# Performance work log

Hardware: AMD Instinct MI355X
Metric: run time of the kernel (lower is better)

Reference implementation:

```python
import jax, jax.numpy as jnp
import numpy as np

N = 100000        # num nodes
E = 1600000       # num edges (no self loops; added inside reference)
F_IN = 501        # dataset.num_features + 1
H1, C1 = 8, 8     # conv1: heads=8, out_channels=8 (concat -> 64)
NCLS = 40         # conv2: heads=1, out_channels=num_classes, concat=False
NEG_SLOPE = 0.2


def _glorot(key, shape):
    fan_in, fan_out = shape[-2] if len(shape) > 1 else shape[-1], shape[-1]
    lim = np.sqrt(6.0 / (fan_in + fan_out)).astype(np.float32)
    return jax.random.uniform(key, shape, jnp.float32, -lim, lim)


def setup_inputs() -> dict:
    key = jax.random.key(0)
    ks = jax.random.split(key, 10)
    x = jax.random.normal(ks[0], (N, F_IN), jnp.float32)
    # random edges guaranteed to have src != dst (PyG removes self loops then re-adds)
    src = jax.random.randint(ks[1], (E,), 0, N)
    off = jax.random.randint(ks[2], (E,), 1, N)
    dst = (src + off) % N
    edge_index = jnp.stack([src, dst]).astype(jnp.int32)
    W1 = _glorot(ks[3], (F_IN, H1 * C1))
    att_src1 = _glorot(ks[4], (H1, C1))
    att_dst1 = _glorot(ks[5], (H1, C1))
    W2 = _glorot(ks[6], (H1 * C1, NCLS))
    att_src2 = _glorot(ks[7], (1, NCLS))
    att_dst2 = _glorot(ks[8], (1, NCLS))
    bias2 = jnp.zeros((NCLS,), jnp.float32)
    return {"x": x, "W1": W1, "att_src1": att_src1, "att_dst1": att_dst1,
            "W2": W2, "att_src2": att_src2, "att_dst2": att_dst2,
            "bias2": bias2, "edge_index": edge_index, "idx": 0}


def _gat_conv(x2d, W, att_s, att_d, src, dst, heads, C, sign, concat, bias):
    n = x2d.shape[0]
    # linear projection (shared lin_src == lin_dst for int in_channels)
    xh = (x2d @ W).reshape(n, heads, C)                       # [N,H,C]
    a_src = jnp.sum(xh * (sign * att_s), axis=-1)             # [N,H]
    a_dst = jnp.sum(xh * (sign * att_d), axis=-1)             # [N,H]
    # add self loops
    ar = jnp.arange(n, dtype=src.dtype)
    src = jnp.concatenate([src, ar])
    dst = jnp.concatenate([dst, ar])
    # per-edge attention logits + leaky relu
    alpha = a_src[src] + a_dst[dst]                           # [E',H]
    alpha = jax.nn.leaky_relu(alpha, NEG_SLOPE)
    # segment softmax grouped by destination node
    m = jax.ops.segment_max(alpha, dst, num_segments=n)       # [N,H]
    e = jnp.exp(alpha - m[dst])
    denom = jax.ops.segment_sum(e, dst, num_segments=n)       # [N,H]
    a = e / (denom[dst] + 1e-16)                              # [E',H]
    # scatter-add aggregation of weighted source features
    out = jax.ops.segment_sum(xh[src] * a[:, :, None], dst, num_segments=n)  # [N,H,C]
    out = out.reshape(n, heads * C) if concat else out.mean(axis=1)
    if bias is not None:
        out = out + bias
    return out


def reference(x, W1, att_src1, att_dst1, W2, att_src2, att_dst2, bias2, edge_index, idx):
    sign = -1.0 if idx == 1 else 1.0
    src, dst = edge_index[0], edge_index[1]
    h = _gat_conv(x, W1, att_src1, att_dst1, src, dst, H1, C1, sign, True, None)
    h = jax.nn.elu(h)
    out = _gat_conv(h, W2, att_src2, att_dst2, src, dst, 1, NCLS, sign, False, bias2)
    return out
```

## Files before the change

### kernel.cpp

```cpp
#include <hip/hip_runtime.h>

#define N_NODES 100000
#define N_EDGES 1600000
#define F_IN    501
#define H1      8
#define C1      8
#define D1      64
#define NCLS    40

#define BSH     9
#define NBUCK   196
#define BINBLK  256

typedef __attribute__((ext_vector_type(8))) short bf16x8;
typedef __attribute__((ext_vector_type(4))) float f32x4;

__device__ __forceinline__ float lrelu(float x) { return x > 0.f ? x : 0.2f * x; }

__device__ __forceinline__ unsigned short f2bf(float f) {
    unsigned u = __float_as_uint(f);
    u += 0x7FFFu + ((u >> 16) & 1u);
    return (unsigned short)(u >> 16);
}
__device__ __forceinline__ float bf2f(unsigned short u) {
    return __uint_as_float(((unsigned)u) << 16);
}

__global__ __launch_bounds__(512) void gemm1(const float* __restrict__ x,
                                             const float* __restrict__ W1,
                                             unsigned short* __restrict__ xh1b) {
    __shared__ unsigned short Bs[64 * 512];

    const int tid = threadIdx.x;

    for (int i = tid; i < F_IN * 64; i += 512) {
        int k = i >> 6, n = i & 63;
        int byte = (n << 10) + (k << 1);
        byte ^= (n & 7) << 4;
        Bs[byte >> 1] = f2bf(W1[i]);
    }
    if (tid < 64) {
        #pragma unroll
        for (int k = F_IN; k < 512; ++k) {
            int byte = (tid << 10) + (k << 1);
            byte ^= (tid & 7) << 4;
            Bs[byte >> 1] = 0;
        }
    }
    __syncthreads();

    const int lane = tid & 63;
    const int wave = tid >> 6;
    const int lr   = lane & 15;
    const int hi   = lane >> 4;
    const int lk   = hi * 8;

    const int row  = blockIdx.x * 128 + wave * 16 + lr;
    const int rowc = row < N_NODES ? row : N_NODES - 1;
    const float* aptr = x + (size_t)rowc * F_IN + lk;

    f32x4 acc[4] = {};
    float av[4][8];

    #pragma unroll
    for (int pf = 0; pf < 4; ++pf)
        #pragma unroll
        for (int j = 0; j < 8; ++j)
            av[pf][j] = aptr[pf * 32 + j];

    #pragma unroll
    for (int s = 0; s < 16; ++s) {
        bf16x8 a;
        #pragma unroll
        for (int j = 0; j < 8; ++j) a[j] = (short)f2bf(av[s & 3][j]);

        if (s + 4 < 15) {
            #pragma unroll
            for (int j = 0; j < 8; ++j)
                av[s & 3][j] = aptr[(s + 4) * 32 + j];
        } else if (s + 4 == 15) {
            #pragma unroll
            for (int j = 0; j < 8; ++j) {
                int k = 15 * 32 + lk + j;
                av[s & 3][j] = (k < F_IN) ? aptr[15 * 32 + j] : 0.f;
            }
        }

        #pragma unroll
        for (int n = 0; n < 4; ++n) {
            int c = n * 16 + lr;
            int byte = (c << 10) + ((s * 32 + lk) << 1);
            byte ^= (c & 7) << 4;
            bf16x8 b = *(const bf16x8*)((const char*)Bs + byte);
            acc[n] = __builtin_amdgcn_mfma_f32_16x16x32_bf16(a, b, acc[n], 0, 0, 0);
        }
    }

    int rbase = blockIdx.x * 128 + wave * 16 + hi * 4;
    #pragma unroll
    for (int n = 0; n < 4; ++n) {
        int col = n * 16 + lr;
        #pragma unroll
        for (int r = 0; r < 4; ++r) {
            int grow = rbase + r;
            if (grow < N_NODES) xh1b[(size_t)grow * D1 + col] = f2bf(acc[n][r]);
        }
    }
}

__global__ void a1k(const unsigned short* __restrict__ xh1b,
                    const float* __restrict__ att_s, const float* __restrict__ att_d,
                    const int* __restrict__ idxp,
                    float* __restrict__ a_src, float* __restrict__ a_dst) {
    int gid = blockIdx.x * blockDim.x + threadIdx.x;
    if (gid >= N_NODES * H1) return;
    int n = gid >> 3, h = gid & 7;
    float sign = (idxp[0] == 1) ? -1.f : 1.f;
    uint4 u = *(const uint4*)(xh1b + (size_t)n * D1 + h * C1);
    float v[8];
    v[0] = bf2f((unsigned short)(u.x & 0xffff)); v[1] = bf2f((unsigned short)(u.x >> 16));
    v[2] = bf2f((unsigned short)(u.y & 0xffff)); v[3] = bf2f((unsigned short)(u.y >> 16));
    v[4] = bf2f((unsigned short)(u.z & 0xffff)); v[5] = bf2f((unsigned short)(u.z >> 16));
    v[6] = bf2f((unsigned short)(u.w & 0xffff)); v[7] = bf2f((unsigned short)(u.w >> 16));
    float ss = 0.f, sd = 0.f;
    #pragma unroll
    for (int c = 0; c < C1; ++c) {
        ss += v[c] * att_s[h * C1 + c];
        sd += v[c] * att_d[h * C1 + c];
    }
    a_src[gid] = sign * ss;
    a_dst[gid] = sign * sd;
}

__global__ __launch_bounds__(256) void bc1(const int* __restrict__ ei,
                                           int* __restrict__ gcnt) {
    __shared__ int h[NBUCK];
    for (int i = threadIdx.x; i < NBUCK; i += 256) h[i] = 0;
    __syncthreads();
    for (int e = blockIdx.x * 256 + threadIdx.x; e < N_EDGES; e += BINBLK * 256)
        atomicAdd(&h[ei[N_EDGES + e] >> BSH], 1);
    __syncthreads();
    for (int i = threadIdx.x; i < NBUCK; i += 256)
        if (h[i]) atomicAdd(&gcnt[i], h[i]);
}

__global__ __launch_bounds__(256) void bc2(const int* __restrict__ gcnt,
                                           int* __restrict__ bbase,
                                           int* __restrict__ bcur,
                                           int* __restrict__ rowptr) {
    __shared__ int s[256];
    int t = threadIdx.x;
    int v = (t < NBUCK) ? gcnt[t] : 0;
    s[t] = v;
    __syncthreads();
    for (int off = 1; off < 256; off <<= 1) {
        int x = 0;
        if (t >= off) x = s[t - off];
        __syncthreads();
        if (t >= off) s[t] += x;
        __syncthreads();
    }
    if (t < NBUCK) { int e = s[t] - v; bbase[t] = e; bcur[t] = e; }
    if (t == 0)    { bbase[NBUCK] = N_EDGES; rowptr[N_NODES] = N_EDGES; }
}

__global__ __launch_bounds__(256) void bc3(const int* __restrict__ ei,
                                           int* __restrict__ bcur,
                                           unsigned* __restrict__ tmp) {
    __shared__ int h[NBUCK];
    __shared__ int base[NBUCK];
    for (int i = threadIdx.x; i < NBUCK; i += 256) h[i] = 0;
    __syncthreads();
    for (int e = blockIdx.x * 256 + threadIdx.x; e < N_EDGES; e += BINBLK * 256)
        atomicAdd(&h[ei[N_EDGES + e] >> BSH], 1);
    __syncthreads();
    for (int i = threadIdx.x; i < NBUCK; i += 256) {
        int c = h[i];
        base[i] = c ? atomicAdd(&bcur[i], c) : 0;
        h[i] = 0;
    }
    __syncthreads();
    for (int e = blockIdx.x * 256 + threadIdx.x; e < N_EDGES; e += BINBLK * 256) {
        int s = ei[e], d = ei[N_EDGES + e];
        int b = d >> BSH;
        int r = atomicAdd(&h[b], 1);
        tmp[base[b] + r] = ((unsigned)s << BSH) | (unsigned)(d & 511);
    }
}

__global__ __launch_bounds__(256) void bc4(const unsigned* __restrict__ tmp,
                                           const int* __restrict__ bbase,
                                           int* __restrict__ rowptr,
                                           int* __restrict__ ssrc) {
    __shared__ int cnt[512], ofs[512], sc[256];
    const int b = blockIdx.x, t = threadIdx.x;
    const int lo = bbase[b], hi = bbase[b + 1];
    cnt[t] = 0; cnt[t + 256] = 0;
    __syncthreads();
    for (int i = lo + t; i < hi; i += 256)
        atomicAdd(&cnt[tmp[i] & 511], 1);
    __syncthreads();
    int v0 = cnt[2 * t], v1 = cnt[2 * t + 1];
    int sum = v0 + v1;
    sc[t] = sum;
    __syncthreads();
    for (int off = 1; off < 256; off <<= 1) {
        int x = 0;
        if (t >= off) x = sc[t - off];
        __syncthreads();
        if (t >= off) sc[t] += x;
        __syncthreads();
    }
    int pre = sc[t] - sum;
    int n0 = (b << BSH) + 2 * t;
    int base0 = lo + pre, base1 = base0 + v0;
    if (n0 < N_NODES)     rowptr[n0]     = base0;
    if (n0 + 1 < N_NODES) rowptr[n0 + 1] = base1;
    ofs[2 * t] = base0; ofs[2 * t + 1] = base1;
    __syncthreads();
    for (int i = lo + t; i < hi; i += 256) {
        unsigned v = tmp[i];
        int p = atomicAdd(&ofs[v & 511], 1);
        ssrc[p] = (int)(v >> BSH);
    }
}

__global__ __launch_bounds__(256) void agg1(const int* __restrict__ rowptr,
                                            const int* __restrict__ ssrc,
                                            const unsigned short* __restrict__ xh1b,
                                            const float* __restrict__ a_src,
                                            const float* __restrict__ a_dst,
                                            unsigned short* __restrict__ hb) {
    int wid  = (blockIdx.x * 256 + threadIdx.x) >> 6;
    int lane = threadIdx.x & 63;
    if (wid >= N_NODES) return;
    const int d  = wid;
    const int li = lane & 15;
    const int q  = lane >> 4;
    const int hh = li >> 1;

    const float adh = a_dst[d * H1 + hh];
    float a0 = 0.f, a1 = 0.f, a2 = 0.f, a3 = 0.f, den = 0.f;
    if (q == 0) {
        float e0 = __expf(lrelu(a_src[d * H1 + hh] + adh));
        ushort4 v = *(const ushort4*)&xh1b[(size_t)d * D1 + (li << 2)];
        a0 = e0 * bf2f(v.x); a1 = e0 * bf2f(v.y);
        a2 = e0 * bf2f(v.z); a3 = e0 * bf2f(v.w);
        den = e0;
    }

    const int beg = rowptr[d], end = rowptr[d + 1];
    for (int p = beg + q; p < end; p += 4) {
        int s = ssrc[p];
        float e = __expf(lrelu(a_src[s * H1 + hh] + adh));
        ushort4 v = *(const ushort4*)&xh1b[(size_t)s * D1 + (li << 2)];
        a0 = fmaf(e, bf2f(v.x), a0);
        a1 = fmaf(e, bf2f(v.y), a1);
        a2 = fmaf(e, bf2f(v.z), a2);
        a3 = fmaf(e, bf2f(v.w), a3);
        den += e;
    }

    a0 += __shfl_xor(a0, 16); a0 += __shfl_xor(a0, 32);
    a1 += __shfl_xor(a1, 16); a1 += __shfl_xor(a1, 32);
    a2 += __shfl_xor(a2, 16); a2 += __shfl_xor(a2, 32);
    a3 += __shfl_xor(a3, 16); a3 += __shfl_xor(a3, 32);
    den += __shfl_xor(den, 16); den += __shfl_xor(den, 32);

    if (lane < 16) {
        float inv = 1.f / (den + 1e-16f);
        float v0 = a0 * inv, v1 = a1 * inv, v2 = a2 * inv, v3 = a3 * inv;
        v0 = v0 > 0.f ? v0 : (__expf(v0) - 1.f);
        v1 = v1 > 0.f ? v1 : (__expf(v1) - 1.f);
        v2 = v2 > 0.f ? v2 : (__expf(v2) - 1.f);
        v3 = v3 > 0.f ? v3 : (__expf(v3) - 1.f);
        ushort4 r;
        r.x = f2bf(v0); r.y = f2bf(v1); r.z = f2bf(v2); r.w = f2bf(v3);
        *(ushort4*)&hb[(size_t)d * D1 + (li << 2)] = r;
    }
}

__global__ void gemm2(const unsigned short* __restrict__ hb,
                      const float* __restrict__ W2,
                      unsigned short* __restrict__ xh2b) {
    int gid = blockIdx.x * blockDim.x + threadIdx.x;
    if (gid >= N_NODES * NCLS) return;
    int n = gid / NCLS, c = gid % NCLS;
    const uint4* hr = (const uint4*)(hb + (size_t)n * D1);
    float s = 0.f;
    #pragma unroll
    for (int q = 0; q < 8; ++q) {
        uint4 u = hr[q];
        int k = q * 8;
        s = fmaf(bf2f((unsigned short)(u.x & 0xffff)), W2[(k + 0) * NCLS + c], s);
        s = fmaf(bf2f((unsigned short)(u.x >> 16)),    W2[(k + 1) * NCLS + c], s);
        s = fmaf(bf2f((unsigned short)(u.y & 0xffff)), W2[(k + 2) * NCLS + c], s);
        s = fmaf(bf2f((unsigned short)(u.y >> 16)),    W2[(k + 3) * NCLS + c], s);
        s = fmaf(bf2f((unsigned short)(u.z & 0xffff)), W2[(k + 4) * NCLS + c], s);
        s = fmaf(bf2f((unsigned short)(u.z >> 16)),    W2[(k + 5) * NCLS + c], s);
        s = fmaf(bf2f((unsigned short)(u.w & 0xffff)), W2[(k + 6) * NCLS + c], s);
        s = fmaf(bf2f((unsigned short)(u.w >> 16)),    W2[(k + 7) * NCLS + c], s);
    }
    xh2b[gid] = f2bf(s);
}

__global__ void a2k(const unsigned short* __restrict__ xh2b,
                    const float* __restrict__ att_s2, const float* __restrict__ att_d2,
                    const int* __restrict__ idxp,
                    float* __restrict__ a_src2, float* __restrict__ a_dst2) {
    int n = blockIdx.x * blockDim.x + threadIdx.x;
    if (n >= N_NODES) return;
    float sign = (idxp[0] == 1) ? -1.f : 1.f;
    const uint4* xr = (const uint4*)(xh2b + (size_t)n * NCLS);
    float ss = 0.f, sd = 0.f;
    #pragma unroll
    for (int q = 0; q < 5; ++q) {
        uint4 u = xr[q];
        int k = q * 8;
        float v[8];
        v[0] = bf2f((unsigned short)(u.x & 0xffff)); v[1] = bf2f((unsigned short)(u.x >> 16));
        v[2] = bf2f((unsigned short)(u.y & 0xffff)); v[3] = bf2f((unsigned short)(u.y >> 16));
        v[4] = bf2f((unsigned short)(u.z & 0xffff)); v[5] = bf2f((unsigned short)(u.z >> 16));
        v[6] = bf2f((unsigned short)(u.w & 0xffff)); v[7] = bf2f((unsigned short)(u.w >> 16));
        #pragma unroll
        for (int j = 0; j < 8; ++j) {
            ss += v[j] * att_s2[k + j];
            sd += v[j] * att_d2[k + j];
        }
    }
    a_src2[n] = sign * ss;
    a_dst2[n] = sign * sd;
}

__global__ __launch_bounds__(256) void agg2(const int* __restrict__ rowptr,
                                            const int* __restrict__ ssrc,
                                            const unsigned short* __restrict__ xh2b,
                                            const float* __restrict__ a_src2,
                                            const float* __restrict__ a_dst2,
                                            const float* __restrict__ bias2,
                                            float* __restrict__ out) {
    int wid  = (blockIdx.x * 256 + threadIdx.x) >> 6;
    int lane = threadIdx.x & 63;
    if (wid >= N_NODES) return;
    const int d  = wid;
    const int li = lane & 15;
    const int q  = lane >> 4;
    const bool act = li < (NCLS / 4);

    const float adh = a_dst2[d];
    float a0 = 0.f, a1 = 0.f, a2 = 0.f, a3 = 0.f, den = 0.f;
    if (q == 0) {
        float e0 = __expf(lrelu(a_src2[d] + adh));
        if (act) {
            ushort4 v = *(const ushort4*)&xh2b[(size_t)d * NCLS + (li << 2)];
            a0 = e0 * bf2f(v.x); a1 = e0 * bf2f(v.y);
            a2 = e0 * bf2f(v.z); a3 = e0 * bf2f(v.w);
        }
        den = e0;
    }

    const int beg = rowptr[d], end = rowptr[d + 1];
    for (int p = beg + q; p < end; p += 4) {
        int s = ssrc[p];
        float e = __expf(lrelu(a_src2[s] + adh));
        if (act) {
            ushort4 v = *(const ushort4*)&xh2b[(size_t)s * NCLS + (li << 2)];
            a0 = fmaf(e, bf2f(v.x), a0);
            a1 = fmaf(e, bf2f(v.y), a1);
            a2 = fmaf(e, bf2f(v.z), a2);
            a3 = fmaf(e, bf2f(v.w), a3);
        }
        den += e;
    }

    a0 += __shfl_xor(a0, 16); a0 += __shfl_xor(a0, 32);
    a1 += __shfl_xor(a1, 16); a1 += __shfl_xor(a1, 32);
    a2 += __shfl_xor(a2, 16); a2 += __shfl_xor(a2, 32);
    a3 += __shfl_xor(a3, 16); a3 += __shfl_xor(a3, 32);
    den += __shfl_xor(den, 16); den += __shfl_xor(den, 32);

    if (lane < 16 && act) {
        float inv = 1.f / (den + 1e-16f);
        float4 bv = *(const float4*)&bias2[li << 2];
        float4 r;
        r.x = a0 * inv + bv.x;
        r.y = a1 * inv + bv.y;
        r.z = a2 * inv + bv.z;
        r.w = a3 * inv + bv.w;
        *(float4*)&out[(size_t)d * NCLS + (li << 2)] = r;
    }
}

extern "C" void kernel_launch(void* const* d_in, const int* in_sizes, int n_in,
                              void* d_out, int out_size, void* d_ws, size_t ws_size,
                              hipStream_t stream) {
    const float* x    = (const float*)d_in[0];
    const float* W1   = (const float*)d_in[1];
    const float* as1w = (const float*)d_in[2];
    const float* ad1w = (const float*)d_in[3];
    const float* W2   = (const float*)d_in[4];
    const float* as2w = (const float*)d_in[5];
    const float* ad2w = (const float*)d_in[6];
    const float* b2   = (const float*)d_in[7];
    const int*   ei   = (const int*)d_in[8];
    const int*   idxp = (const int*)d_in[9];
    float* out = (float*)d_out;

    unsigned short* xh1b = (unsigned short*)d_ws;
    unsigned short* hb   = xh1b + (size_t)N_NODES * D1;
    unsigned short* xh2b = hb + (size_t)N_NODES * D1;
    float* as1 = (float*)(xh2b + (size_t)N_NODES * NCLS);
    float* ad1 = as1 + (size_t)N_NODES * H1;
    float* as2 = ad1 + (size_t)N_NODES * H1;
    float* ad2 = as2 + N_NODES;
    int* gcnt   = (int*)(ad2 + N_NODES);
    int* bbase  = gcnt + NBUCK;
    int* bcur   = bbase + (NBUCK + 1);
    int* rowptr = bcur + NBUCK;
    unsigned* tmp = (unsigned*)(rowptr + (N_NODES + 1));
    int* ssrc   = (int*)(tmp + N_EDGES);

    hipMemsetAsync(gcnt, 0, (size_t)NBUCK * sizeof(int), stream);
    bc1<<<BINBLK, 256, 0, stream>>>(ei, gcnt);
    bc2<<<1, 256, 0, stream>>>(gcnt, bbase, bcur, rowptr);
    bc3<<<BINBLK, 256, 0, stream>>>(ei, bcur, tmp);
    bc4<<<NBUCK, 256, 0, stream>>>(tmp, bbase, rowptr, ssrc);

    gemm1<<<(N_NODES + 127) / 128, 512, 0, stream>>>(x, W1, xh1b);
    a1k<<<(N_NODES * H1 + 255) / 256, 256, 0, stream>>>(xh1b, as1w, ad1w, idxp, as1, ad1);
    agg1<<<(N_NODES * 64 + 255) / 256, 256, 0, stream>>>(rowptr, ssrc, xh1b, as1, ad1, hb);

    gemm2<<<(N_NODES * NCLS + 255) / 256, 256, 0, stream>>>(hb, W2, xh2b);
    a2k<<<(N_NODES + 255) / 256, 256, 0, stream>>>(xh2b, as2w, ad2w, idxp, as2, ad2);
    agg2<<<(N_NODES * 64 + 255) / 256, 256, 0, stream>>>(rowptr, ssrc, xh2b, as2, ad2, b2, out);
}
```

Measured before the change: 336.2 us.

## Partition node features into channel planes and aggregate each plane in separate passes

```diff
diff --git a/kernel.cpp b/kernel.cpp
--- a/kernel.cpp
+++ b/kernel.cpp
@@ -28,7 +28,7 @@
 
 __global__ __launch_bounds__(512) void gemm1(const float* __restrict__ x,
                                              const float* __restrict__ W1,
-                                             unsigned short* __restrict__ xh1b) {
+                                             unsigned short* __restrict__ xh1p) {
     __shared__ unsigned short Bs[64 * 512];
 
     const int tid = threadIdx.x;
@@ -99,24 +99,28 @@
     int rbase = blockIdx.x * 128 + wave * 16 + hi * 4;
     #pragma unroll
     for (int n = 0; n < 4; ++n) {
-        int col = n * 16 + lr;
+        unsigned short* dst = xh1p + (size_t)n * N_NODES * 16;
         #pragma unroll
         for (int r = 0; r < 4; ++r) {
             int grow = rbase + r;
-            if (grow < N_NODES) xh1b[(size_t)grow * D1 + col] = f2bf(acc[n][r]);
+            if (grow < N_NODES) dst[(size_t)grow * 16 + lr] = f2bf(acc[n][r]);
         }
     }
 }
 
-__global__ void a1k(const unsigned short* __restrict__ xh1b,
+__global__ void a1k(const unsigned short* __restrict__ xh1p,
                     const float* __restrict__ att_s, const float* __restrict__ att_d,
                     const int* __restrict__ idxp,
-                    float* __restrict__ a_src, float* __restrict__ a_dst) {
+                    float* __restrict__ asP, float* __restrict__ adP) {
     int gid = blockIdx.x * blockDim.x + threadIdx.x;
-    if (gid >= N_NODES * H1) return;
-    int n = gid >> 3, h = gid & 7;
+    if (gid >= 4 * 2 * N_NODES) return;
+    int p   = gid / (2 * N_NODES);
+    int r   = gid - p * (2 * N_NODES);
+    int n   = r >> 1, sub = r & 1;
+    int h   = 2 * p + sub;
     float sign = (idxp[0] == 1) ? -1.f : 1.f;
-    uint4 u = *(const uint4*)(xh1b + (size_t)n * D1 + h * C1);
+    const unsigned short* row = xh1p + (size_t)p * N_NODES * 16 + n * 16 + sub * 8;
+    uint4 u = *(const uint4*)row;
     float v[8];
     v[0] = bf2f((unsigned short)(u.x & 0xffff)); v[1] = bf2f((unsigned short)(u.x >> 16));
     v[2] = bf2f((unsigned short)(u.y & 0xffff)); v[3] = bf2f((unsigned short)(u.y >> 16));
@@ -124,12 +128,12 @@
     v[6] = bf2f((unsigned short)(u.w & 0xffff)); v[7] = bf2f((unsigned short)(u.w >> 16));
     float ss = 0.f, sd = 0.f;
     #pragma unroll
-    for (int c = 0; c < C1; ++c) {
+    for (int c = 0; c < 8; ++c) {
         ss += v[c] * att_s[h * C1 + c];
         sd += v[c] * att_d[h * C1 + c];
     }
-    a_src[gid] = sign * ss;
-    a_dst[gid] = sign * sd;
+    asP[gid] = sign * ss;
+    adP[gid] = sign * sd;
 }
 
 __global__ __launch_bounds__(256) void bc1(const int* __restrict__ ei,
@@ -225,35 +229,39 @@
     }
 }
 
-__global__ __launch_bounds__(256) void agg1(const int* __restrict__ rowptr,
-                                            const int* __restrict__ ssrc,
-                                            const unsigned short* __restrict__ xh1b,
-                                            const float* __restrict__ a_src,
-                                            const float* __restrict__ a_dst,
-                                            unsigned short* __restrict__ hb) {
+__global__ __launch_bounds__(256) void agg1p(const int* __restrict__ rowptr,
+                                             const int* __restrict__ ssrc,
+                                             const unsigned short* __restrict__ xp,
+                                             const float2* __restrict__ asp,
+                                             const float2* __restrict__ adp,
+                                             unsigned short* __restrict__ hb,
+                                             int chbase) {
     int wid  = (blockIdx.x * 256 + threadIdx.x) >> 6;
     int lane = threadIdx.x & 63;
     if (wid >= N_NODES) return;
-    const int d  = wid;
-    const int li = lane & 15;
-    const int q  = lane >> 4;
-    const int hh = li >> 1;
-
-    const float adh = a_dst[d * H1 + hh];
+    const int d     = wid;
+    const int li    = lane & 3;
+    const int chain = lane >> 2;
+    const int hsel  = li >> 1;
+
+    float2 adv = adp[d];
+    const float adh = hsel ? adv.y : adv.x;
     float a0 = 0.f, a1 = 0.f, a2 = 0.f, a3 = 0.f, den = 0.f;
-    if (q == 0) {
-        float e0 = __expf(lrelu(a_src[d * H1 + hh] + adh));
-        ushort4 v = *(const ushort4*)&xh1b[(size_t)d * D1 + (li << 2)];
+    if (chain == 0) {
+        float2 asd = asp[d];
+        float e0 = __expf(lrelu((hsel ? asd.y : asd.x) + adh));
+        ushort4 v = *(const ushort4*)&xp[(size_t)d * 16 + (li << 2)];
         a0 = e0 * bf2f(v.x); a1 = e0 * bf2f(v.y);
         a2 = e0 * bf2f(v.z); a3 = e0 * bf2f(v.w);
         den = e0;
     }
 
     const int beg = rowptr[d], end = rowptr[d + 1];
-    for (int p = beg + q; p < end; p += 4) {
+    for (int p = beg + chain; p < end; p += 16) {
         int s = ssrc[p];
-        float e = __expf(lrelu(a_src[s * H1 + hh] + adh));
-        ushort4 v = *(const ushort4*)&xh1b[(size_t)s * D1 + (li << 2)];
+        float2 asv = asp[s];
+        ushort4 v = *(const ushort4*)&xp[(size_t)s * 16 + (li << 2)];
+        float e = __expf(lrelu((hsel ? asv.y : asv.x) + adh));
         a0 = fmaf(e, bf2f(v.x), a0);
         a1 = fmaf(e, bf2f(v.y), a1);
         a2 = fmaf(e, bf2f(v.z), a2);
@@ -261,13 +269,16 @@
         den += e;
     }
 
-    a0 += __shfl_xor(a0, 16); a0 += __shfl_xor(a0, 32);
-    a1 += __shfl_xor(a1, 16); a1 += __shfl_xor(a1, 32);
-    a2 += __shfl_xor(a2, 16); a2 += __shfl_xor(a2, 32);
-    a3 += __shfl_xor(a3, 16); a3 += __shfl_xor(a3, 32);
-    den += __shfl_xor(den, 16); den += __shfl_xor(den, 32);
-
-    if (lane < 16) {
+    #pragma unroll
+    for (int m = 4; m <= 32; m <<= 1) {
+        a0 += __shfl_xor(a0, m);
+        a1 += __shfl_xor(a1, m);
+        a2 += __shfl_xor(a2, m);
+        a3 += __shfl_xor(a3, m);
+        den += __shfl_xor(den, m);
+    }
+
+    if (lane < 4) {
         float inv = 1.f / (den + 1e-16f);
         float v0 = a0 * inv, v1 = a1 * inv, v2 = a2 * inv, v3 = a3 * inv;
         v0 = v0 > 0.f ? v0 : (__expf(v0) - 1.f);
@@ -276,13 +287,15 @@
         v3 = v3 > 0.f ? v3 : (__expf(v3) - 1.f);
         ushort4 r;
         r.x = f2bf(v0); r.y = f2bf(v1); r.z = f2bf(v2); r.w = f2bf(v3);
-        *(ushort4*)&hb[(size_t)d * D1 + (li << 2)] = r;
+        *(ushort4*)&hb[(size_t)d * D1 + chbase + (li << 2)] = r;
     }
 }
 
 __global__ void gemm2(const unsigned short* __restrict__ hb,
                       const float* __restrict__ W2,
-                      unsigned short* __restrict__ xh2b) {
+                      unsigned short* __restrict__ xa,
+                      unsigned short* __restrict__ xb,
+                      unsigned short* __restrict__ xc) {
     int gid = blockIdx.x * blockDim.x + threadIdx.x;
     if (gid >= N_NODES * NCLS) return;
     int n = gid / NCLS, c = gid % NCLS;
@@ -301,93 +314,161 @@
         s = fmaf(bf2f((unsigned short)(u.w & 0xffff)), W2[(k + 6) * NCLS + c], s);
         s = fmaf(bf2f((unsigned short)(u.w >> 16)),    W2[(k + 7) * NCLS + c], s);
     }
-    xh2b[gid] = f2bf(s);
-}
-
-__global__ void a2k(const unsigned short* __restrict__ xh2b,
+    unsigned short bv = f2bf(s);
+    if (c < 16)      xa[(size_t)n * 16 + c]        = bv;
+    else if (c < 32) xb[(size_t)n * 16 + (c - 16)] = bv;
+    else             xc[(size_t)n * 8  + (c - 32)] = bv;
+}
+
+__global__ void a2k(const unsigned short* __restrict__ xa,
+                    const unsigned short* __restrict__ xb,
+                    const unsigned short* __restrict__ xc,
                     const float* __restrict__ att_s2, const float* __restrict__ att_d2,
                     const int* __restrict__ idxp,
                     float* __restrict__ a_src2, float* __restrict__ a_dst2) {
     int n = blockIdx.x * blockDim.x + threadIdx.x;
     if (n >= N_NODES) return;
     float sign = (idxp[0] == 1) ? -1.f : 1.f;
-    const uint4* xr = (const uint4*)(xh2b + (size_t)n * NCLS);
     float ss = 0.f, sd = 0.f;
     #pragma unroll
-    for (int q = 0; q < 5; ++q) {
-        uint4 u = xr[q];
-        int k = q * 8;
-        float v[8];
-        v[0] = bf2f((unsigned short)(u.x & 0xffff)); v[1] = bf2f((unsigned short)(u.x >> 16));
-        v[2] = bf2f((unsigned short)(u.y & 0xffff)); v[3] = bf2f((unsigned short)(u.y >> 16));
-        v[4] = bf2f((unsigned short)(u.z & 0xffff)); v[5] = bf2f((unsigned short)(u.z >> 16));
-        v[6] = bf2f((unsigned short)(u.w & 0xffff)); v[7] = bf2f((unsigned short)(u.w >> 16));
-        #pragma unroll
-        for (int j = 0; j < 8; ++j) {
-            ss += v[j] * att_s2[k + j];
-            sd += v[j] * att_d2[k + j];
+    for (int part = 0; part < 3; ++part) {
+        const unsigned short* base = part == 0 ? xa + (size_t)n * 16
+                                   : part == 1 ? xb + (size_t)n * 16
+                                               : xc + (size_t)n * 8;
+        int nch = part == 2 ? 8 : 16;
+        int c0  = part * 16;
+        for (int q = 0; q < nch / 8; ++q) {
+            uint4 u = *(const uint4*)(base + q * 8);
+            float v[8];
+            v[0] = bf2f((unsigned short)(u.x & 0xffff)); v[1] = bf2f((unsigned short)(u.x >> 16));
+            v[2] = bf2f((unsigned short)(u.y & 0xffff)); v[3] = bf2f((unsigned short)(u.y >> 16));
+            v[4] = bf2f((unsigned short)(u.z & 0xffff)); v[5] = bf2f((unsigned short)(u.z >> 16));
+            v[6] = bf2f((unsigned short)(u.w & 0xffff)); v[7] = bf2f((unsigned short)(u.w >> 16));
+            #pragma unroll
+            for (int j = 0; j < 8; ++j) {
+                int c = c0 + q * 8 + j;
+                ss += v[j] * att_s2[c];
+                sd += v[j] * att_d2[c];
+            }
         }
     }
     a_src2[n] = sign * ss;
     a_dst2[n] = sign * sd;
 }
 
-__global__ __launch_bounds__(256) void agg2(const int* __restrict__ rowptr,
-                                            const int* __restrict__ ssrc,
-                                            const unsigned short* __restrict__ xh2b,
-                                            const float* __restrict__ a_src2,
-                                            const float* __restrict__ a_dst2,
-                                            const float* __restrict__ bias2,
-                                            float* __restrict__ out) {
+__global__ __launch_bounds__(256) void agg2p16(const int* __restrict__ rowptr,
+                                               const int* __restrict__ ssrc,
+                                               const unsigned short* __restrict__ xp,
+                                               const float* __restrict__ as2,
+                                               const float* __restrict__ ad2,
+                                               const float* __restrict__ bias2,
+                                               float* __restrict__ out, int cbase) {
     int wid  = (blockIdx.x * 256 + threadIdx.x) >> 6;
     int lane = threadIdx.x & 63;
     if (wid >= N_NODES) return;
-    const int d  = wid;
-    const int li = lane & 15;
-    const int q  = lane >> 4;
-    const bool act = li < (NCLS / 4);
-
-    const float adh = a_dst2[d];
+    const int d     = wid;
+    const int li    = lane & 3;
+    const int chain = lane >> 2;
+
+    const float adh = ad2[d];
     float a0 = 0.f, a1 = 0.f, a2 = 0.f, a3 = 0.f, den = 0.f;
-    if (q == 0) {
-        float e0 = __expf(lrelu(a_src2[d] + adh));
-        if (act) {
-            ushort4 v = *(const ushort4*)&xh2b[(size_t)d * NCLS + (li << 2)];
-            a0 = e0 * bf2f(v.x); a1 = e0 * bf2f(v.y);
-            a2 = e0 * bf2f(v.z); a3 = e0 * bf2f(v.w);
-        }
+    if (chain == 0) {
+        float e0 = __expf(lrelu(as2[d] + adh));
+        ushort4 v = *(const ushort4*)&xp[(size_t)d * 16 + (li << 2)];
+        a0 = e0 * bf2f(v.x); a1 = e0 * bf2f(v.y);
+        a2 = e0 * bf2f(v.z); a3 = e0 * bf2f(v.w);
         den = e0;
     }
 
     const int beg = rowptr[d], end = rowptr[d + 1];
-    for (int p = beg + q; p < end; p += 4) {
+    for (int p = beg + chain; p < end; p += 16) {
         int s = ssrc[p];
-        float e = __expf(lrelu(a_src2[s] + adh));
-        if (act) {
-            ushort4 v = *(const ushort4*)&xh2b[(size_t)s * NCLS + (li << 2)];
-            a0 = fmaf(e, bf2f(v.x), a0);
-            a1 = fmaf(e, bf2f(v.y), a1);
-            a2 = fmaf(e, bf2f(v.z), a2);
-            a3 = fmaf(e, bf2f(v.w), a3);
-        }
+        float as = as2[s];
+        ushort4 v = *(const ushort4*)&xp[(size_t)s * 16 + (li << 2)];
+        float e = __expf(lrelu(as + adh));
+        a0 = fmaf(e, bf2f(v.x), a0);
+        a1 = fmaf(e, bf2f(v.y), a1);
+        a2 = fmaf(e, bf2f(v.z), a2);
+        a3 = fmaf(e, bf2f(v.w), a3);
         den += e;
     }
 
-    a0 += __shfl_xor(a0, 16); a0 += __shfl_xor(a0, 32);
-    a1 += __shfl_xor(a1, 16); a1 += __shfl_xor(a1, 32);
-    a2 += __shfl_xor(a2, 16); a2 += __shfl_xor(a2, 32);
-    a3 += __shfl_xor(a3, 16); a3 += __shfl_xor(a3, 32);
-    den += __shfl_xor(den, 16); den += __shfl_xor(den, 32);
-
-    if (lane < 16 && act) {
+    #pragma unroll
+    for (int m = 4; m <= 32; m <<= 1) {
+        a0 += __shfl_xor(a0, m);
+        a1 += __shfl_xor(a1, m);
+        a2 += __shfl_xor(a2, m);
+        a3 += __shfl_xor(a3, m);
+        den += __shfl_xor(den, m);
+    }
+
+    if (lane < 4) {
         float inv = 1.f / (den + 1e-16f);
-        float4 bv = *(const float4*)&bias2[li << 2];
+        const float* bp = bias2 + cbase + (li << 2);
         float4 r;
-        r.x = a0 * inv + bv.x;
-        r.y = a1 * inv + bv.y;
-        r.z = a2 * inv + bv.z;
-        r.w = a3 * inv + bv.w;
-        *(float4*)&out[(size_t)d * NCLS + (li << 2)] = r;
+        r.x = a0 * inv + bp[0];
+        r.y = a1 * inv + bp[1];
+        r.z = a2 * inv + bp[2];
+        r.w = a3 * inv + bp[3];
+        *(float4*)&out[(size_t)d * NCLS + cbase + (li << 2)] = r;
+    }
+}
+
+__global__ __launch_bounds__(256) void agg2p8(const int* __restrict__ rowptr,
+                                              const int* __restrict__ ssrc,
+                                              const unsigned short* __restrict__ xp,
+                                              const float* __restrict__ as2,
+                                              const float* __restrict__ ad2,
+                                              const float* __restrict__ bias2,
+                                              float* __restrict__ out) {
+    int wid  = (blockIdx.x * 256 + threadIdx.x) >> 6;
+    int lane = threadIdx.x & 63;
+    if (wid >= N_NODES) return;
+    const int d     = wid;
+    const int li    = lane & 1;
+    const int chain = lane >> 1;
+
+    const float adh = ad2[d];
+    float a0 = 0.f, a1 = 0.f, a2 = 0.f, a3 = 0.f, den = 0.f;
+    if (chain == 0) {
+        float e0 = __expf(lrelu(as2[d] + adh));
+        ushort4 v = *(const ushort4*)&xp[(size_t)d * 8 + (li << 2)];
+        a0 = e0 * bf2f(v.x); a1 = e0 * bf2f(v.y);
+        a2 = e0 * bf2f(v.z); a3 = e0 * bf2f(v.w);
+        den = e0;
+    }
+
+    const int beg = rowptr[d], end = rowptr[d + 1];
+    for (int p = beg + chain; p < end; p += 32) {
+        int s = ssrc[p];
+        float as = as2[s];
+        ushort4 v = *(const ushort4*)&xp[(size_t)s * 8 + (li << 2)];
+        float e = __expf(lrelu(as + adh));
+        a0 = fmaf(e, bf2f(v.x), a0);
+        a1 = fmaf(e, bf2f(v.y), a1);
+        a2 = fmaf(e, bf2f(v.z), a2);
+        a3 = fmaf(e, bf2f(v.w), a3);
+        den += e;
+    }
+
+    #pragma unroll
+    for (int m = 2; m <= 32; m <<= 1) {
+        a0 += __shfl_xor(a0, m);
+        a1 += __shfl_xor(a1, m);
+        a2 += __shfl_xor(a2, m);
+        a3 += __shfl_xor(a3, m);
+        den += __shfl_xor(den, m);
+    }
+
+    if (lane < 2) {
+        float inv = 1.f / (den + 1e-16f);
+        const float* bp = bias2 + 32 + (li << 2);
+        float4 r;
+        r.x = a0 * inv + bp[0];
+        r.y = a1 * inv + bp[1];
+        r.z = a2 * inv + bp[2];
+        r.w = a3 * inv + bp[3];
+        *(float4*)&out[(size_t)d * NCLS + 32 + (li << 2)] = r;
     }
 }
 
@@ -406,12 +487,14 @@
     const int*   idxp = (const int*)d_in[9];
     float* out = (float*)d_out;
 
-    unsigned short* xh1b = (unsigned short*)d_ws;
-    unsigned short* hb   = xh1b + (size_t)N_NODES * D1;
-    unsigned short* xh2b = hb + (size_t)N_NODES * D1;
-    float* as1 = (float*)(xh2b + (size_t)N_NODES * NCLS);
-    float* ad1 = as1 + (size_t)N_NODES * H1;
-    float* as2 = ad1 + (size_t)N_NODES * H1;
+    unsigned short* xh1p = (unsigned short*)d_ws;
+    unsigned short* hb   = xh1p + (size_t)4 * N_NODES * 16;
+    unsigned short* xa   = hb + (size_t)N_NODES * D1;
+    unsigned short* xb   = xa + (size_t)N_NODES * 16;
+    unsigned short* xc   = xb + (size_t)N_NODES * 16;
+    float* asP = (float*)(xc + (size_t)N_NODES * 8);
+    float* adP = asP + (size_t)8 * N_NODES;
+    float* as2 = adP + (size_t)8 * N_NODES;
     float* ad2 = as2 + N_NODES;
     int* gcnt   = (int*)(ad2 + N_NODES);
     int* bbase  = gcnt + NBUCK;
@@ -426,11 +509,20 @@
     bc3<<<BINBLK, 256, 0, stream>>>(ei, bcur, tmp);
     bc4<<<NBUCK, 256, 0, stream>>>(tmp, bbase, rowptr, ssrc);
 
-    gemm1<<<(N_NODES + 127) / 128, 512, 0, stream>>>(x, W1, xh1b);
-    a1k<<<(N_NODES * H1 + 255) / 256, 256, 0, stream>>>(xh1b, as1w, ad1w, idxp, as1, ad1);
-    agg1<<<(N_NODES * 64 + 255) / 256, 256, 0, stream>>>(rowptr, ssrc, xh1b, as1, ad1, hb);
-
-    gemm2<<<(N_NODES * NCLS + 255) / 256, 256, 0, stream>>>(hb, W2, xh2b);
-    a2k<<<(N_NODES + 255) / 256, 256, 0, stream>>>(xh2b, as2w, ad2w, idxp, as2, ad2);
-    agg2<<<(N_NODES * 64 + 255) / 256, 256, 0, stream>>>(rowptr, ssrc, xh2b, as2, ad2, b2, out);
-}
+    gemm1<<<(N_NODES + 127) / 128, 512, 0, stream>>>(x, W1, xh1p);
+    a1k<<<(4 * 2 * N_NODES + 255) / 256, 256, 0, stream>>>(xh1p, as1w, ad1w, idxp, asP, adP);
+    const int GAGG = (N_NODES * 64 + 255) / 256;
+    for (int p = 0; p < 4; ++p) {
+        agg1p<<<GAGG, 256, 0, stream>>>(rowptr, ssrc,
+                                        xh1p + (size_t)p * N_NODES * 16,
+                                        (const float2*)(asP + (size_t)p * 2 * N_NODES),
+                                        (const float2*)(adP + (size_t)p * 2 * N_NODES),
+                                        hb, p * 16);
+    }
+
+    gemm2<<<(N_NODES * NCLS + 255) / 256, 256, 0, stream>>>(hb, W2, xa, xb, xc);
+    a2k<<<(N_NODES + 255) / 256, 256, 0, stream>>>(xa, xb, xc, as2w, ad2w, idxp, as2, ad2);
+    agg2p16<<<GAGG, 256, 0, stream>>>(rowptr, ssrc, xa, as2, ad2, b2, out, 0);
+    agg2p16<<<GAGG, 256, 0, stream>>>(rowptr, ssrc, xb, as2, ad2, b2, out, 16);
+    agg2p8 <<<GAGG, 256, 0, stream>>>(rowptr, ssrc, xc, as2, ad2, b2, out);
+}
```

New measurement: 454.7 us. 1.35x slower.
